# Performance work log

Measured on AMD Instinct MI355X. Metric: run time of the kernel, lower is better.

## Reference

```python
import jax, jax.numpy as jnp
import numpy as np
import math

B, SQ, SKV = 8, 1024, 1024
D, H, DQ, DV = 1024, 16, 64, 64
EPS = 1e-3  # Keras LayerNormalization default epsilon
IN_DECODER = True


def _layer_norm(x, gamma, beta):
    m = jnp.mean(x, axis=-1, keepdims=True)
    v = jnp.mean((x - m) ** 2, axis=-1, keepdims=True)
    return gamma * (x - m) / jnp.sqrt(v + EPS) + beta


def setup_inputs() -> dict:
    key = jax.random.key(0)
    ks = jax.random.split(key, 6)
    x = jax.random.normal(ks[0], (B, SQ, D), dtype=jnp.float32)
    # self-attention: query and key/value sequences are the same tensor
    lengths = jax.random.randint(ks[1], (B,), SKV // 2, SKV + 1, dtype=jnp.int32)
    init = 0.02
    Wq = jax.random.normal(ks[2], (D, H * DQ), dtype=jnp.float32) * init
    Wkv = jax.random.normal(ks[3], (D, H * (DQ + DV)), dtype=jnp.float32) * init
    Wo = jax.random.normal(ks[4], (H * DV, D), dtype=jnp.float32) * init
    return {
        "query_sequences": x,
        "key_value_sequences": x,
        "key_value_sequence_lengths": lengths,
        "Wq": Wq, "bq": jnp.zeros((H * DQ,), jnp.float32),
        "Wkv": Wkv, "bkv": jnp.zeros((H * (DQ + DV),), jnp.float32),
        "Wo": Wo, "bo": jnp.zeros((D,), jnp.float32),
        "ln_gamma": jnp.ones((D,), jnp.float32),
        "ln_beta": jnp.zeros((D,), jnp.float32),
    }


def reference(query_sequences, key_value_sequences, key_value_sequence_lengths,
              Wq, bq, Wkv, bkv, Wo, bo, ln_gamma, ln_beta):
    # detect self-attention exactly as the original (elementwise equality)
    self_attn = jnp.all(query_sequences == key_value_sequences)
    q_seq = _layer_norm(query_sequences, ln_gamma, ln_beta)
    kv_ln = _layer_norm(key_value_sequences, ln_gamma, ln_beta)
    kv_seq = jnp.where(self_attn, kv_ln, key_value_sequences)
    residual = q_seq  # pre-norm residual (original adds post-LN queries)

    q = (q_seq @ Wq + bq).reshape(B, SQ, H, DQ).transpose(0, 2, 1, 3)   # b h q d
    kvp = kv_seq @ Wkv + bkv
    k = kvp[..., : H * DQ].reshape(B, SKV, H, DQ).transpose(0, 2, 1, 3)  # b h k d
    v = kvp[..., H * DQ:].reshape(B, SKV, H, DV).transpose(0, 2, 1, 3)   # b h k d

    scores = jnp.einsum("bhqd,bhkd->bhqk", q, k) / math.sqrt(DQ)
    # padding mask on keys
    not_pad = (jnp.arange(SKV)[None, None, None, :]
               < key_value_sequence_lengths[:, None, None, None])
    scores = jnp.where(not_pad, scores, -jnp.inf)
    if IN_DECODER:
        causal = jnp.tril(jnp.ones((SQ, SKV), dtype=bool))[None, None]
        scores = jnp.where(jnp.logical_or(~self_attn, causal), scores, -jnp.inf)

    attn = jax.nn.softmax(scores, axis=-1)  # dropout is identity in eval mode
    out = jnp.einsum("bhqk,bhkd->bhqd", attn, v)
    out = out.transpose(0, 2, 1, 3).reshape(B, SQ, H * DV)
    out = out @ Wo + bo
    return out + residual
```

## Files before the change

kernel.cpp:

```cpp
#include <hip/hip_runtime.h>

typedef unsigned short u16;
typedef unsigned int u32;
typedef __attribute__((ext_vector_type(8))) short short8;
typedef __attribute__((ext_vector_type(4))) float fx4;

#define LOG2E 1.44269504088896340736f

__device__ __forceinline__ u16 f2bf(float f) {
    unsigned int u = __float_as_uint(f);
    u += 0x7fffu + ((u >> 16) & 1u);
    return (u16)(u >> 16);
}

__device__ __forceinline__ float bf2f(u16 v) {
    u32 u = ((u32)v) << 16;
    return __uint_as_float(u);
}

__device__ __forceinline__ u32 pack_bf2(float lo, float hi) {
    return __builtin_amdgcn_perm(__float_as_uint(hi), __float_as_uint(lo), 0x07060302u);
}

__device__ __forceinline__ float fast_exp2(float x) {
#if __has_builtin(__builtin_amdgcn_exp2f)
    return __builtin_amdgcn_exp2f(x);
#else
    return exp2f(x);
#endif
}

__device__ __forceinline__ fx4 mfma16(short8 a, short8 b, fx4 c) {
    return __builtin_amdgcn_mfma_f32_16x16x32_bf16(a, b, c, 0, 0, 0);
}

__device__ __forceinline__ void gload_lds16(const u16* g, u16* l) {
    __builtin_amdgcn_global_load_lds(
        (const __attribute__((address_space(1))) void*)g,
        (__attribute__((address_space(3))) void*)l, 16, 0, 0);
}

__global__ __launch_bounds__(256) void ln_wt_kernel(
    const float* __restrict__ x, const float* __restrict__ gamma,
    const float* __restrict__ beta, u16* __restrict__ yb,
    const float* __restrict__ Wq, const float* __restrict__ Wkv,
    const float* __restrict__ Wo, u16* __restrict__ Wt) {
    int blk = blockIdx.x;
    if (blk < 2048) {
        int wave = threadIdx.x >> 6, lane = threadIdx.x & 63;
        int row = (blk << 2) + wave;
        const float* xr = x + ((size_t)row << 10);
        float4 v[4];
        float s = 0.0f, sq = 0.0f;
#pragma unroll
        for (int i = 0; i < 4; ++i) {
            v[i] = *(const float4*)(xr + (i << 8) + (lane << 2));
            s  += v[i].x + v[i].y + v[i].z + v[i].w;
            sq += v[i].x * v[i].x + v[i].y * v[i].y + v[i].z * v[i].z + v[i].w * v[i].w;
        }
#pragma unroll
        for (int o = 32; o > 0; o >>= 1) {
            s  += __shfl_xor(s, o, 64);
            sq += __shfl_xor(sq, o, 64);
        }
        float mean = s * (1.0f / 1024.0f);
        float var  = sq * (1.0f / 1024.0f) - mean * mean;
        float rstd = rsqrtf(var + 1e-3f);
#pragma unroll
        for (int i = 0; i < 4; ++i) {
            int off = (i << 8) + (lane << 2);
            float4 g  = *(const float4*)(gamma + off);
            float4 bb = *(const float4*)(beta + off);
            float4 y;
            y.x = (v[i].x - mean) * rstd * g.x + bb.x;
            y.y = (v[i].y - mean) * rstd * g.y + bb.y;
            y.z = (v[i].z - mean) * rstd * g.z + bb.z;
            y.w = (v[i].w - mean) * rstd * g.w + bb.w;
            unsigned long long p = (unsigned long long)f2bf(y.x)
                | ((unsigned long long)f2bf(y.y) << 16)
                | ((unsigned long long)f2bf(y.z) << 32)
                | ((unsigned long long)f2bf(y.w) << 48);
            *(unsigned long long*)(yb + ((size_t)row << 10) + off) = p;
        }
    } else {
        int wtb = blk - 2048;
        int n0 = (wtb & 127) << 5;
        int k0 = (wtb >> 7) << 5;
        const float* W; int sn0, SN;
        if (n0 < 1024)      { W = Wq;  sn0 = n0;        SN = 1024; }
        else if (n0 < 3072) { W = Wkv; sn0 = n0 - 1024; SN = 2048; }
        else                { W = Wo;  sn0 = n0 - 3072; SN = 1024; }
        __shared__ float tile[32][33];
        int tx = threadIdx.x & 31, ty = threadIdx.x >> 5;
#pragma unroll
        for (int r = 0; r < 4; ++r)
            tile[ty + r * 8][tx] = W[(size_t)(k0 + ty + r * 8) * SN + sn0 + tx];
        __syncthreads();
#pragma unroll
        for (int r = 0; r < 4; ++r)
            Wt[(size_t)(n0 + ty + r * 8) * 1024 + k0 + tx] = f2bf(tile[tx][ty + r * 8]);
    }
}

template <int MODE, int WMT>
__global__ __launch_bounds__(256) void gemm_bt(
    const u16* __restrict__ A, const u16* __restrict__ Bt,
    const float* __restrict__ bq, const float* __restrict__ bkv,
    const u16* __restrict__ resb, float* __restrict__ Cf, u16* __restrict__ Cb,
    u16* __restrict__ Vt, int M, int N, int K, float qscale) {
    __shared__ __align__(16) u16 sA[WMT * 32 * 64];
    __shared__ __align__(16) u16 sB[128 * 64];
    int m0 = blockIdx.y * (WMT * 32), n0 = blockIdx.x << 7;
    int tid = threadIdx.x, lane = tid & 63, wave = tid >> 6;
    int quad = lane >> 4, l15 = lane & 15, swr = lane & 7;
    int wm = (wave >> 1) * (WMT * 16), wn = (wave & 1) << 6;
    int srow = lane >> 3;
    int gseg = (lane & 7) ^ srow;

    fx4 acc[WMT][4];
    fx4 zero = {0.0f, 0.0f, 0.0f, 0.0f};
#pragma unroll
    for (int i = 0; i < WMT; ++i)
#pragma unroll
        for (int j = 0; j < 4; ++j) acc[i][j] = zero;

    for (int k0 = 0; k0 < K; k0 += 64) {
#pragma unroll
        for (int t = 0; t < WMT; ++t) {
            int cA = wave * WMT + t;
            int rowA = (cA << 3) + srow;
            gload_lds16(A + (size_t)(m0 + rowA) * K + k0 + (gseg << 3), &sA[cA << 9]);
            if (t < 4) {
                int cB = (wave << 2) + t;
                int rowB = (cB << 3) + srow;
                gload_lds16(Bt + (size_t)(n0 + rowB) * K + k0 + (gseg << 3), &sB[cB << 9]);
            }
        }
        __syncthreads();
#pragma unroll
        for (int kk = 0; kk < 64; kk += 32) {
            int ks = (kk >> 3) + quad;
            short8 af[WMT], bf[4];
#pragma unroll
            for (int mt = 0; mt < WMT; ++mt) {
                int r = wm + (mt << 4) + l15;
                af[mt] = *(const short8*)&sA[(r << 6) + (((ks ^ swr) & 7) << 3)];
            }
#pragma unroll
            for (int nt = 0; nt < 4; ++nt) {
                int r = wn + (nt << 4) + l15;
                bf[nt] = *(const short8*)&sB[(r << 6) + (((ks ^ swr) & 7) << 3)];
            }
#pragma unroll
            for (int mt = 0; mt < WMT; ++mt)
#pragma unroll
                for (int nt = 0; nt < 4; ++nt)
                    acc[mt][nt] = mfma16(af[mt], bf[nt], acc[mt][nt]);
        }
        __syncthreads();
    }

    if (MODE == 0 && n0 >= 2048) {
#pragma unroll
        for (int mt = 0; mt < WMT; ++mt)
#pragma unroll
            for (int nt = 0; nt < 4; ++nt)
#pragma unroll
                for (int r = 0; r < 4; ++r) {
                    int row = m0 + wm + (mt << 4) + (quad << 2) + r;
                    int col = n0 + wn + (nt << 4) + l15;
                    float v = acc[mt][nt][r] + bkv[col - 1024];
                    int bb = row >> 10, k = row & 1023;
                    int h = (col - 2048) >> 6, d = col & 63;
                    int kt = k >> 6, kin = k & 63;
                    int kp = ((kin & 15) << 2) | (kin >> 4);
                    Vt[(size_t)((((bb << 4) + h) << 6) + d) * 1024
                       + (kt << 6) + kp] = f2bf(v);
                }
        return;
    }

#pragma unroll
    for (int mt = 0; mt < WMT; ++mt)
#pragma unroll
        for (int nt = 0; nt < 4; ++nt)
#pragma unroll
            for (int r = 0; r < 4; ++r) {
                int row = m0 + wm + (mt << 4) + (quad << 2) + r;
                int col = n0 + wn + (nt << 4) + l15;
                if (MODE == 1) {
                    float v = acc[mt][nt][r] + bq[col];
                    size_t idx = (size_t)row * N + col;
                    Cf[idx] = v + bf2f(resb[idx]);
                } else {
                    float bias = (col < 1024) ? bq[col] : bkv[col - 1024];
                    float v = acc[mt][nt][r] + bias;
                    if (col < 1024) v *= qscale;
                    Cb[(size_t)row * N + col] = f2bf(v);
                }
            }
}

__global__ __launch_bounds__(256) void attn_kernel(
    const u16* __restrict__ QKVp, const u16* __restrict__ Vt,
    const int* __restrict__ lens, u16* __restrict__ O) {
    int bh = blockIdx.x;
    int b = bh >> 4, h = bh & 15;
    int j = blockIdx.y;
    int len = lens[b];
    int cap = (len - 1) >> 6;
    int tid = threadIdx.x, lane = tid & 63, w = tid >> 6;
    int quad = lane >> 4, l15 = lane & 15;

    __shared__ __align__(16) u16 sK[64 * 64];
    __shared__ __align__(16) u16 sV[64 * 64];
    __shared__ __align__(16) u16 sP[4 * 2048];
    u16* sPw = &sP[w << 11];

    int lrow = lane >> 3;
    int lseg = lane & 7;

    fx4 zero = {0.0f, 0.0f, 0.0f, 0.0f};

#pragma unroll
    for (int phase = 0; phase < 2; ++phase) {
        int s = phase ? (7 - j) : j;
        int q0 = s << 7;
        int wq0 = q0 + (w << 5);
        int ktend_blk = min((q0 + 127) >> 6, cap);
        int ktend_w   = min((wq0 + 31) >> 6, cap);

        short8 qf[2][2];
#pragma unroll
        for (int mt = 0; mt < 2; ++mt)
#pragma unroll
            for (int kk = 0; kk < 2; ++kk) {
                int qrow = (b << 10) + wq0 + (mt << 4) + l15;
                qf[mt][kk] = *(const short8*)(QKVp + (size_t)qrow * 3072
                              + (h << 6) + (kk << 5) + (quad << 3));
            }

        fx4 oacc[2][4];
        float lsum[2][4];
#pragma unroll
        for (int mt = 0; mt < 2; ++mt)
#pragma unroll
            for (int nt = 0; nt < 4; ++nt) oacc[mt][nt] = zero;
#pragma unroll
        for (int mt = 0; mt < 2; ++mt)
#pragma unroll
            for (int r = 0; r < 4; ++r) lsum[mt][r] = 0.0f;

        for (int kt = 0; kt <= ktend_blk; ++kt) {
            int k0g = kt << 6;
#pragma unroll
            for (int i = 0; i < 2; ++i) {
                int row = (w << 4) + (i << 3) + lrow;
                int gs = lseg ^ (row & 7);
                gload_lds16(QKVp + (size_t)((b << 10) + k0g + row) * 3072
                               + 1024 + (h << 6) + (gs << 3),
                            &sK[((w << 1) + i) << 9]);
                gload_lds16(Vt + (size_t)((bh << 6) + row) * 1024
                               + k0g + (gs << 3),
                            &sV[((w << 1) + i) << 9]);
            }
            __syncthreads();

            if (kt <= ktend_w) {
                fx4 sacc[2][4];
#pragma unroll
                for (int mt = 0; mt < 2; ++mt)
#pragma unroll
                    for (int nt = 0; nt < 4; ++nt) sacc[mt][nt] = zero;
#pragma unroll
                for (int kk = 0; kk < 2; ++kk) {
                    int seg = (kk << 2) + quad;
                    short8 kf[4];
#pragma unroll
                    for (int nt = 0; nt < 4; ++nt) {
                        int row = (nt << 4) + l15;
                        kf[nt] = *(const short8*)&sK[(row << 6)
                                   + (((seg ^ (row & 7)) & 7) << 3)];
                    }
#pragma unroll
                    for (int mt = 0; mt < 2; ++mt)
#pragma unroll
                        for (int nt = 0; nt < 4; ++nt)
                            sacc[mt][nt] = mfma16(qf[mt][kk], kf[nt], sacc[mt][nt]);
                }

                bool needm = ((k0g + 63) > wq0) || ((k0g + 64) > len);
                if (needm) {
#pragma unroll
                    for (int mt = 0; mt < 2; ++mt)
#pragma unroll
                        for (int nt = 0; nt < 4; ++nt) {
                            int kg = k0g + (nt << 4) + l15;
#pragma unroll
                            for (int r = 0; r < 4; ++r) {
                                int qr = wq0 + (mt << 4) + (quad << 2) + r;
                                if (kg > qr || kg >= len)
                                    sacc[mt][nt][r] = -30000.0f;
                            }
                        }
                }

#pragma unroll
                for (int mt = 0; mt < 2; ++mt) {
#pragma unroll
                    for (int nt = 0; nt < 4; ++nt)
#pragma unroll
                        for (int r = 0; r < 4; ++r)
                            sacc[mt][nt][r] = fast_exp2(sacc[mt][nt][r]);
#pragma unroll
                    for (int r = 0; r < 4; ++r) {
                        lsum[mt][r] += (sacc[mt][0][r] + sacc[mt][1][r])
                                     + (sacc[mt][2][r] + sacc[mt][3][r]);
                        int row = (mt << 4) + (quad << 2) + r;
                        u32 lo = pack_bf2(sacc[mt][0][r], sacc[mt][1][r]);
                        u32 hi = pack_bf2(sacc[mt][2][r], sacc[mt][3][r]);
                        uint2 pv; pv.x = lo; pv.y = hi;
                        int addr = (row << 6)
                                 + (((((l15 >> 1)) ^ (row & 7)) & 7) << 3)
                                 + ((l15 & 1) << 2);
                        *(uint2*)&sPw[addr] = pv;
                    }
                }
                __builtin_amdgcn_s_waitcnt(0xC07F);

#pragma unroll
                for (int kk = 0; kk < 2; ++kk) {
                    int seg = (kk << 2) + quad;
                    short8 vf[4], pf[2];
#pragma unroll
                    for (int nt = 0; nt < 4; ++nt) {
                        int row = (nt << 4) + l15;
                        vf[nt] = *(const short8*)&sV[(row << 6)
                                   + (((seg ^ (row & 7)) & 7) << 3)];
                    }
#pragma unroll
                    for (int mt = 0; mt < 2; ++mt) {
                        int row = (mt << 4) + l15;
                        pf[mt] = *(const short8*)&sPw[(row << 6)
                                   + (((seg ^ (row & 7)) & 7) << 3)];
                    }
#pragma unroll
                    for (int mt = 0; mt < 2; ++mt)
#pragma unroll
                        for (int nt = 0; nt < 4; ++nt)
                            oacc[mt][nt] = mfma16(pf[mt], vf[nt], oacc[mt][nt]);
                }
            }
            __syncthreads();
        }

#pragma unroll
        for (int mt = 0; mt < 2; ++mt)
#pragma unroll
            for (int r = 0; r < 4; ++r) {
                float v = lsum[mt][r];
                v += __shfl_xor(v, 1, 64);
                v += __shfl_xor(v, 2, 64);
                v += __shfl_xor(v, 4, 64);
                v += __shfl_xor(v, 8, 64);
                lsum[mt][r] = __builtin_amdgcn_rcpf(v);
            }
#pragma unroll
        for (int mt = 0; mt < 2; ++mt)
#pragma unroll
            for (int nt = 0; nt < 4; ++nt)
#pragma unroll
                for (int r = 0; r < 4; ++r) {
                    int row = (b << 10) + wq0 + (mt << 4) + (quad << 2) + r;
                    int col = (h << 6) + (nt << 4) + l15;
                    O[((size_t)row << 10) + col] =
                        f2bf(oacc[mt][nt][r] * lsum[mt][r]);
                }
    }
}

extern "C" void kernel_launch(void* const* d_in, const int* in_sizes, int n_in,
                              void* d_out, int out_size, void* d_ws, size_t ws_size,
                              hipStream_t stream) {
    (void)in_sizes; (void)n_in; (void)out_size; (void)ws_size;
    const float* x    = (const float*)d_in[0];
    const int*   lens = (const int*)d_in[2];
    const float* Wq   = (const float*)d_in[3];
    const float* bq   = (const float*)d_in[4];
    const float* Wkv  = (const float*)d_in[5];
    const float* bkv  = (const float*)d_in[6];
    const float* Wo   = (const float*)d_in[7];
    const float* bo   = (const float*)d_in[8];
    const float* gam  = (const float*)d_in[9];
    const float* bet  = (const float*)d_in[10];
    float* out = (float*)d_out;

    char* w = (char*)d_ws;
    u16* xln_b  = (u16*)w;  w += (size_t)8192 * 1024 * 2;
    u16* Wall_t = (u16*)w;  w += (size_t)4096 * 1024 * 2;
    u16* QKVp   = (u16*)w;  w += (size_t)8192 * 3072 * 2;
    u16* Vt     = (u16*)w;  w += (size_t)8192 * 1024 * 2;
    u16* AO     = (u16*)w;  w += (size_t)8192 * 1024 * 2;

    ln_wt_kernel<<<6144, 256, 0, stream>>>(x, gam, bet, xln_b, Wq, Wkv, Wo, Wall_t);
    gemm_bt<0, 4><<<dim3(24, 64), 256, 0, stream>>>(xln_b, Wall_t, bq, bkv,
        nullptr, nullptr, QKVp, Vt, 8192, 3072, 1024, 0.125f * LOG2E);
    attn_kernel<<<dim3(128, 4), 256, 0, stream>>>(QKVp, Vt, lens, AO);
    gemm_bt<1, 4><<<dim3(8, 64), 256, 0, stream>>>(AO, Wall_t + (size_t)3072 * 1024,
        bo, nullptr, xln_b, out, nullptr, nullptr, 8192, 1024, 1024, 1.0f);
}
```

Before: 259.4 us.

## Add 256x256-tile 8-wave QKV projection GEMM with quarter-phase LDS pipelining

Replaces the 128x128 QKV projection GEMM with a dedicated kernel that uses 512 threads and 256x256 output tiles. It double-buffers LDS, issuing half-tile prefetches interleaved across four compute phases with explicit waitcnt, barriers and setprio around the MFMA bursts. A grid swizzle improves L2 locality. The larger tile raises arithmetic intensity per loaded byte, but it uses 128 KB of LDS and many accumulator registers per thread, which may limit occupancy.

```diff
diff --git a/kernel.cpp b/kernel.cpp
--- a/kernel.cpp
+++ b/kernel.cpp
@@ -100,6 +100,134 @@
         for (int r = 0; r < 4; ++r)
             Wt[(size_t)(n0 + ty + r * 8) * 1024 + k0 + tx] = f2bf(tile[tx][ty + r * 8]);
     }
+}
+
+__global__ __launch_bounds__(512, 2) void gemm_qkv8(
+    const u16* __restrict__ A, const u16* __restrict__ Bt,
+    const float* __restrict__ bq, const float* __restrict__ bkv,
+    u16* __restrict__ Cb, u16* __restrict__ Vt, float qscale) {
+    __shared__ __align__(16) u16 sA[2][256 * 64];
+    __shared__ __align__(16) u16 sB[2][256 * 64];
+
+    int id = blockIdx.x;
+    int swz = (id & 7) * 48 + (id >> 3);
+    int mtile = swz / 12, ntile = swz - mtile * 12;
+    int m0 = mtile << 8, n0 = ntile << 8;
+
+    int tid = threadIdx.x, lane = tid & 63, wave = tid >> 6;
+    int quad = lane >> 4, l15 = lane & 15;
+    int srow = lane >> 3, gseg = (lane & 7) ^ srow;
+    int wm = wave >> 2, wn = wave & 3;
+
+    fx4 acc[8][4];
+    fx4 zero = {0.0f, 0.0f, 0.0f, 0.0f};
+#pragma unroll
+    for (int i = 0; i < 8; ++i)
+#pragma unroll
+        for (int j = 0; j < 4; ++j) acc[i][j] = zero;
+
+    auto stA = [&](int kt, int half, int b) {
+#pragma unroll
+        for (int rnd = 0; rnd < 2; ++rnd) {
+            int lr = (half << 7) + (((rnd << 3) + wave) << 3);
+            gload_lds16(A + (size_t)(m0 + lr + srow) * 1024 + (kt << 6) + (gseg << 3),
+                        &sA[b][lr << 6]);
+        }
+    };
+    auto stB = [&](int kt, int half, int b) {
+#pragma unroll
+        for (int rnd = 0; rnd < 2; ++rnd) {
+            int lr = (half << 7) + (((rnd << 3) + wave) << 3);
+            gload_lds16(Bt + (size_t)(n0 + lr + srow) * 1024 + (kt << 6) + (gseg << 3),
+                        &sB[b][lr << 6]);
+        }
+    };
+
+    const int NT = 16;
+
+    stA(0, 0, 0); stA(0, 1, 0); stB(0, 0, 0); stB(0, 1, 0);
+    stA(1, 0, 1); stB(1, 0, 1);
+    asm volatile("s_waitcnt vmcnt(4)" ::: "memory");
+    __syncthreads();
+
+#define PHASE(QM, QN, STAGE, VMW)                                            \
+    do {                                                                     \
+        short8 afr[4][2], bfr[2][2];                                         \
+        _Pragma("unroll") for (int j = 0; j < 4; ++j) {                      \
+            int r = ((QM) << 7) + (wm << 6) + (j << 4) + l15;                \
+            _Pragma("unroll") for (int kk = 0; kk < 2; ++kk)                 \
+                afr[j][kk] = *(const short8*)&sAc[(r << 6) +                 \
+                    ((((kk << 2) + quad) ^ (r & 7)) << 3)];                  \
+        }                                                                    \
+        _Pragma("unroll") for (int n = 0; n < 2; ++n) {                      \
+            int r = ((QN) << 7) + (wn << 5) + (n << 4) + l15;                \
+            _Pragma("unroll") for (int kk = 0; kk < 2; ++kk)                 \
+                bfr[n][kk] = *(const short8*)&sBc[(r << 6) +                 \
+                    ((((kk << 2) + quad) ^ (r & 7)) << 3)];                  \
+        }                                                                    \
+        STAGE;                                                               \
+        VMW;                                                                 \
+        __builtin_amdgcn_s_barrier();                                        \
+        asm volatile("s_waitcnt lgkmcnt(0)" ::: "memory");                   \
+        __builtin_amdgcn_sched_barrier(0);                                   \
+        __builtin_amdgcn_s_setprio(1);                                       \
+        _Pragma("unroll") for (int kk = 0; kk < 2; ++kk)                     \
+            _Pragma("unroll") for (int j = 0; j < 4; ++j)                    \
+                _Pragma("unroll") for (int n = 0; n < 2; ++n)                \
+                    acc[((QM) << 2) + j][((QN) << 1) + n] = mfma16(          \
+                        afr[j][kk], bfr[n][kk],                              \
+                        acc[((QM) << 2) + j][((QN) << 1) + n]);              \
+        __builtin_amdgcn_s_setprio(0);                                       \
+        __builtin_amdgcn_s_barrier();                                        \
+    } while (0)
+
+#pragma unroll 2
+    for (int t = 0; t < NT; ++t) {
+        int cur = t & 1, nxt = cur ^ 1;
+        bool s1 = (t + 1 < NT), s2 = (t + 2 < NT);
+        const u16* sAc = sA[cur];
+        const u16* sBc = sB[cur];
+        PHASE(0, 0, { if (s1) stA(t + 1, 1, nxt); }, {});
+        PHASE(0, 1, { if (s1) stB(t + 1, 1, nxt); }, {});
+        PHASE(1, 0, { if (s2) stA(t + 2, 0, cur); }, {});
+        PHASE(1, 1, { if (s2) stB(t + 2, 0, cur); }, {
+            if (s1) {
+                if (s2) asm volatile("s_waitcnt vmcnt(4)" ::: "memory");
+                else    asm volatile("s_waitcnt vmcnt(0)" ::: "memory");
+            }
+        });
+    }
+#undef PHASE
+
+    bool vregion = (n0 >= 2048);
+#pragma unroll
+    for (int jm = 0; jm < 8; ++jm)
+#pragma unroll
+        for (int jn = 0; jn < 4; ++jn) {
+            int colb = n0 + ((jn & 2) << 6) + (wn << 5) + ((jn & 1) << 4) + l15;
+            int rowb = m0 + ((jm & 4) << 5) + (wm << 6) + ((jm & 3) << 4) + (quad << 2);
+            if (!vregion) {
+                float bias = (colb < 1024) ? bq[colb] : bkv[colb - 1024];
+#pragma unroll
+                for (int r = 0; r < 4; ++r) {
+                    float v = acc[jm][jn][r] + bias;
+                    if (colb < 1024) v *= qscale;
+                    Cb[(size_t)(rowb + r) * 3072 + colb] = f2bf(v);
+                }
+            } else {
+                float bias = bkv[colb - 1024];
+                int h = (colb - 2048) >> 6, d = colb & 63;
+#pragma unroll
+                for (int r = 0; r < 4; ++r) {
+                    int row = rowb + r;
+                    int bb = row >> 10, k = row & 1023;
+                    int kt2 = k >> 6, kin = k & 63;
+                    int kp = ((kin & 15) << 2) | (kin >> 4);
+                    Vt[(size_t)((((bb << 4) + h) << 6) + d) * 1024
+                       + (kt2 << 6) + kp] = f2bf(acc[jm][jn][r] + bias);
+                }
+            }
+        }
 }
 
 template <int MODE, int WMT>
@@ -403,8 +531,8 @@
     u16* AO     = (u16*)w;  w += (size_t)8192 * 1024 * 2;
 
     ln_wt_kernel<<<6144, 256, 0, stream>>>(x, gam, bet, xln_b, Wq, Wkv, Wo, Wall_t);
-    gemm_bt<0, 4><<<dim3(24, 64), 256, 0, stream>>>(xln_b, Wall_t, bq, bkv,
-        nullptr, nullptr, QKVp, Vt, 8192, 3072, 1024, 0.125f * LOG2E);
+    gemm_qkv8<<<384, 512, 0, stream>>>(xln_b, Wall_t, bq, bkv, QKVp, Vt,
+                                       0.125f * LOG2E);
     attn_kernel<<<dim3(128, 4), 256, 0, stream>>>(QKVp, Vt, lens, AO);
     gemm_bt<1, 4><<<dim3(8, 64), 256, 0, stream>>>(AO, Wall_t + (size_t)3072 * 1024,
         bo, nullptr, xln_b, out, nullptr, nullptr, 8192, 1024, 1024, 1.0f);
```

After: 294.7 us. 1.14x slower.
